# Kernel tuning notes

Hardware: AMD Instinct MI355X
Metric: run time of the kernel (lower is better)

The kernel has to match this reference:

```python
import jax, jax.numpy as jnp
import numpy as np

SEQ_LEN = 4096
N_FEATURES = 2048
N_HIDDEN = 2048
TAGS = 10
START_TAG = 8
STOP_TAG = 9
H = N_HIDDEN // 2  # per-direction hidden size


def setup_inputs() -> dict:
    key = jax.random.key(0)
    ks = jax.random.split(key, 10)
    s = 0.02
    sentence = jax.random.normal(ks[0], (SEQ_LEN, 1, N_FEATURES), jnp.float32)
    W_ih_f = jax.random.normal(ks[1], (4 * H, N_FEATURES), jnp.float32) * s
    W_hh_f = jax.random.normal(ks[2], (4 * H, H), jnp.float32) * s
    b_f = jax.random.normal(ks[3], (4 * H,), jnp.float32) * s
    W_ih_b = jax.random.normal(ks[4], (4 * H, N_FEATURES), jnp.float32) * s
    W_hh_b = jax.random.normal(ks[5], (4 * H, H), jnp.float32) * s
    b_b = jax.random.normal(ks[6], (4 * H,), jnp.float32) * s
    W_lin = jax.random.normal(ks[7], (TAGS, N_HIDDEN), jnp.float32) * s
    b_lin = jax.random.normal(ks[8], (TAGS,), jnp.float32) * s
    transitions = jax.random.normal(ks[9], (TAGS, TAGS), jnp.float32)
    transitions = transitions.at[START_TAG, :].set(-10000.0).at[:, STOP_TAG].set(-10000.0)
    return {"sentence": sentence, "W_ih_f": W_ih_f, "W_hh_f": W_hh_f, "b_f": b_f,
            "W_ih_b": W_ih_b, "W_hh_b": W_hh_b, "b_b": b_b,
            "W_lin": W_lin, "b_lin": b_lin, "transitions": transitions}


def _lstm_dir(x, W_ih, W_hh, b, reverse):
    # Precompute the input projection for all timesteps (one big GEMM).
    xp = jnp.einsum('tbf,gf->tbg', x, W_ih) + b  # [T, B, 4H]
    B = x.shape[1]
    init = (jnp.zeros((B, H), x.dtype), jnp.zeros((B, H), x.dtype))

    def step(carry, g):
        h, c = carry
        gates = g + h @ W_hh.T  # [B, 4H], PyTorch gate order i, f, g, o
        i, f, gg, o = jnp.split(gates, 4, axis=-1)
        c = jax.nn.sigmoid(f) * c + jax.nn.sigmoid(i) * jnp.tanh(gg)
        h = jax.nn.sigmoid(o) * jnp.tanh(c)
        return (h, c), h

    _, hs = jax.lax.scan(step, init, xp, reverse=reverse)
    return hs  # [T, B, H]


def reference(sentence, W_ih_f, W_hh_f, b_f, W_ih_b, W_hh_b, b_b, W_lin, b_lin, transitions):
    h_f = _lstm_dir(sentence, W_ih_f, W_hh_f, b_f, False)
    h_b = _lstm_dir(sentence, W_ih_b, W_hh_b, b_b, True)
    lstm_out = jnp.concatenate([h_f, h_b], axis=-1)         # [T, 1, N_HIDDEN]
    feats = lstm_out @ W_lin.T + b_lin                       # [T, 1, TAGS]
    f = feats[:, 0, :]                                       # [T, TAGS] (batch=1 as in original)

    init_v = jnp.full((TAGS,), -10000.0, f.dtype).at[START_TAG].set(0.0)

    def vstep(fv, feat):
        scores = fv[None, :] + transitions                   # [next_tag, prev_tag]
        return jnp.max(scores, axis=1) + feat, jnp.argmax(scores, axis=1)

    fv, bps = jax.lax.scan(vstep, init_v, f)                 # bps: [T, TAGS]
    terminal = fv + transitions[STOP_TAG]
    path_score = jnp.max(terminal)
    best_last = jnp.argmax(terminal)

    def bstep(tag, bp):
        return bp[tag], tag

    _, best_path = jax.lax.scan(bstep, best_last, bps, reverse=True)  # [T] in time order
    return path_score, best_path
```

## Files before the change

kernel.cpp:

```cpp
#include <hip/hip_runtime.h>

typedef _Float16 f16;
typedef _Float16 f16x4 __attribute__((ext_vector_type(4)));
typedef _Float16 f16x8 __attribute__((ext_vector_type(8)));
typedef float f32x4 __attribute__((ext_vector_type(4)));
typedef unsigned u32x4 __attribute__((ext_vector_type(4)));

#define SEQ 4096
#define NF  2048
#define HID 1024

__device__ f16   g_Ahi[SEQ * NF];
__device__ f16   g_Alo[SEQ * NF];
__device__ f16   g_Whi[2 * 4096 * NF];
__device__ f16   g_Wlo[2 * 4096 * NF];
__device__ float g_xp [2u * SEQ * 4096u];
__device__ float g_hist[2u * SEQ * HID];
__device__ unsigned long long g_ring[2][2][1024];
__device__ float g_feats[SEQ * 10];

__global__ void cvt_split(const float* __restrict__ src, int which, int n4) {
  int i = blockIdx.x * blockDim.x + threadIdx.x;
  int stride = gridDim.x * blockDim.x;
  f16* hi; f16* lo;
  if (which == 0)      { hi = g_Ahi; lo = g_Alo; }
  else if (which == 1) { hi = g_Whi; lo = g_Wlo; }
  else                 { hi = g_Whi + 4096 * NF; lo = g_Wlo + 4096 * NF; }
  const float4* s4 = (const float4*)src;
  f16x4* h4 = (f16x4*)hi;
  f16x4* l4 = (f16x4*)lo;
  for (int idx = i; idx < n4; idx += stride) {
    float4 v = s4[idx];
    f16x4 h, l;
    h.x = (f16)v.x; l.x = (f16)(v.x - (float)h.x);
    h.y = (f16)v.y; l.y = (f16)(v.y - (float)h.y);
    h.z = (f16)v.z; l.z = (f16)(v.z - (float)h.z);
    h.w = (f16)v.w; l.w = (f16)(v.w - (float)h.w);
    h4[idx] = h; l4[idx] = l;
  }
}

__global__ __launch_bounds__(256, 1) void gemm_xp(
    const float* __restrict__ b_f, const float* __restrict__ b_b)
{
  const int d = blockIdx.z;
  const f16* WhiD = g_Whi + (size_t)d * (4096u * 2048u);
  const f16* WloD = g_Wlo + (size_t)d * (4096u * 2048u);
  const float* bias = d ? b_b : b_f;
  float* out = g_xp + (size_t)d * (4096u * 4096u);

  __shared__ f16 sAh[128 * 40];
  __shared__ f16 sAl[128 * 40];
  __shared__ f16 sWh[128 * 40];
  __shared__ f16 sWl[128 * 40];

  const int tid  = threadIdx.x;
  const int lane = tid & 63;
  const int wv   = tid >> 6;
  const int quad = lane >> 4;
  const int mrow = lane & 15;
  const int m0 = (wv & 1) * 64;
  const int n0 = (wv >> 1) * 64;
  const int bm = blockIdx.y, bn = blockIdx.x;

  f32x4 acc[4][4] = {};

  const int r0  = tid >> 2;
  const int seg = tid & 3;

  for (int kt = 0; kt < 2048; kt += 32) {
#pragma unroll
    for (int r = 0; r < 2; ++r) {
      int row = r * 64 + r0;
      size_t ga = (size_t)(bm * 128 + row) * 2048 + kt + seg * 8;
      size_t gw = (size_t)(bn * 128 + row) * 2048 + kt + seg * 8;
      int lidx = row * 40 + seg * 8;
      *(f16x8*)&sAh[lidx] = *(const f16x8*)&g_Ahi[ga];
      *(f16x8*)&sAl[lidx] = *(const f16x8*)&g_Alo[ga];
      *(f16x8*)&sWh[lidx] = *(const f16x8*)&WhiD[gw];
      *(f16x8*)&sWl[lidx] = *(const f16x8*)&WloD[gw];
    }
    __syncthreads();

    f16x8 ah[4], al[4], wh[4], wl[4];
#pragma unroll
    for (int mi = 0; mi < 4; ++mi) {
      int rowm = (m0 + mi * 16 + mrow) * 40 + quad * 8;
      ah[mi] = *(const f16x8*)&sAh[rowm];
      al[mi] = *(const f16x8*)&sAl[rowm];
    }
#pragma unroll
    for (int ni = 0; ni < 4; ++ni) {
      int rown = (n0 + ni * 16 + mrow) * 40 + quad * 8;
      wh[ni] = *(const f16x8*)&sWh[rown];
      wl[ni] = *(const f16x8*)&sWl[rown];
    }
#pragma unroll
    for (int mi = 0; mi < 4; ++mi)
#pragma unroll
      for (int ni = 0; ni < 4; ++ni) {
        acc[mi][ni] = __builtin_amdgcn_mfma_f32_16x16x32_f16(ah[mi], wh[ni], acc[mi][ni], 0, 0, 0);
        acc[mi][ni] = __builtin_amdgcn_mfma_f32_16x16x32_f16(ah[mi], wl[ni], acc[mi][ni], 0, 0, 0);
        acc[mi][ni] = __builtin_amdgcn_mfma_f32_16x16x32_f16(al[mi], wh[ni], acc[mi][ni], 0, 0, 0);
      }
    __syncthreads();
  }

#pragma unroll
  for (int ni = 0; ni < 4; ++ni) {
    int g = bn * 128 + n0 + ni * 16 + mrow;
    float bv = bias[g];
#pragma unroll
    for (int mi = 0; mi < 4; ++mi) {
#pragma unroll
      for (int r = 0; r < 4; ++r) {
        int t = bm * 128 + m0 + mi * 16 + quad * 4 + r;
        out[(size_t)t * 4096 + g] = acc[mi][ni][r] + bv;
      }
    }
  }
}

__global__ void init_sync() {
  int i = blockIdx.x * blockDim.x + threadIdx.x;
  ((unsigned long long*)g_ring)[i] = 0ull;
}

__global__ __launch_bounds__(1024) void lstm_persistent(
    const float* __restrict__ Whh_f, const float* __restrict__ Whh_b)
{
  const int bid = blockIdx.x;
  const int dir = bid & 1;
  const int wsl = bid >> 1;
  const int tid = threadIdx.x;
  const int r   = tid >> 4;
  const int l16 = tid & 15;

  __shared__ float h_lds[1024];
  __shared__ float gates_lds[64];

  const float* Wd = dir ? Whh_b : Whh_f;

  const int grow = (r >> 4) * 1024 + wsl * 16 + (r & 15);
  float4 w4[16];
#pragma unroll
  for (int j = 0; j < 16; ++j)
    w4[j] = *(const float4*)&Wd[(size_t)grow * 1024 + 4 * l16 + 64 * j];

  const float* xpd = g_xp + (size_t)dir * 4096u * 4096u;
  float* histd = g_hist + (size_t)dir * 4096u * 1024u;

  float c = 0.f;

  for (int t = 1; t <= 4096; ++t) {
    const int tau = dir ? (4096 - t) : (t - 1);

    float xv0 = 0.f, xv1 = 0.f, xv2 = 0.f, xv3 = 0.f;
    if (tid < 16) {
      const float* px = xpd + (size_t)tau * 4096 + wsl * 16 + tid;
      xv0 = px[0]; xv1 = px[1024]; xv2 = px[2048]; xv3 = px[3072];
    }

    if (tid < 512) {
      const unsigned need = (unsigned)(t - 1);
      const unsigned long long* rs = &g_ring[dir][(t - 1) & 1][0] + 2 * tid;
      u32x4 q;
      for (;;) {
        asm volatile("global_load_dwordx4 %0, %1, off sc0 sc1\n\t"
                     "s_waitcnt vmcnt(0)"
                     : "=v"(q) : "v"(rs) : "memory");
        if (q.y == need && q.w == need) break;
        __builtin_amdgcn_s_sleep(1);
      }
      float2 hv;
      hv.x = __uint_as_float(q.x);
      hv.y = __uint_as_float(q.z);
      *(float2*)&h_lds[2 * tid] = hv;
    }
    __syncthreads();

    float p0 = 0.f, p1 = 0.f, p2 = 0.f, p3 = 0.f;
#pragma unroll
    for (int j = 0; j < 16; j += 4) {
      float4 h0 = *(const float4*)&h_lds[4 * l16 + 64 * (j + 0)];
      float4 h1 = *(const float4*)&h_lds[4 * l16 + 64 * (j + 1)];
      float4 h2 = *(const float4*)&h_lds[4 * l16 + 64 * (j + 2)];
      float4 h3 = *(const float4*)&h_lds[4 * l16 + 64 * (j + 3)];
      p0 += w4[j+0].x*h0.x + w4[j+0].y*h0.y + w4[j+0].z*h0.z + w4[j+0].w*h0.w;
      p1 += w4[j+1].x*h1.x + w4[j+1].y*h1.y + w4[j+1].z*h1.z + w4[j+1].w*h1.w;
      p2 += w4[j+2].x*h2.x + w4[j+2].y*h2.y + w4[j+2].z*h2.z + w4[j+2].w*h2.w;
      p3 += w4[j+3].x*h3.x + w4[j+3].y*h3.y + w4[j+3].z*h3.z + w4[j+3].w*h3.w;
    }
    float acc = (p0 + p1) + (p2 + p3);
    acc += __shfl_xor(acc, 1);
    acc += __shfl_xor(acc, 2);
    acc += __shfl_xor(acc, 4);
    acc += __shfl_xor(acc, 8);
    if (l16 == 0) gates_lds[r] = acc;
    __syncthreads();

    if (tid < 16) {
      float gi = gates_lds[tid]      + xv0;
      float gf = gates_lds[16 + tid] + xv1;
      float gg = gates_lds[32 + tid] + xv2;
      float go = gates_lds[48 + tid] + xv3;
      float si = 1.f / (1.f + __expf(-gi));
      float sf = 1.f / (1.f + __expf(-gf));
      float so = 1.f / (1.f + __expf(-go));
      float tg = 1.f - 2.f / (1.f + __expf(2.f * gg));
      c = sf * c + si * tg;
      float th = 1.f - 2.f / (1.f + __expf(2.f * c));
      float h  = so * th;
      histd[(size_t)tau * 1024 + wsl * 16 + tid] = h;
      unsigned long long pk = ((unsigned long long)(unsigned)t << 32)
                            | (unsigned long long)__float_as_uint(h);
      __hip_atomic_store(&g_ring[dir][t & 1][wsl * 16 + tid], pk,
                         __ATOMIC_RELAXED, __HIP_MEMORY_SCOPE_AGENT);
    }
  }
}

__global__ __launch_bounds__(256, 1) void feats_kernel(
    const float* __restrict__ W_lin, const float* __restrict__ b_lin)
{
  const int tid = threadIdx.x;
  const int wv = tid >> 6, l = tid & 63;
  const int t0 = blockIdx.x * 16 + wv * 4;
  for (int it = 0; it < 4; ++it) {
    const int t = t0 + it;
    float hf[16], hbv[16];
#pragma unroll
    for (int i = 0; i < 16; ++i) hf[i]  = g_hist[(size_t)t * 1024 + l + 64 * i];
#pragma unroll
    for (int i = 0; i < 16; ++i) hbv[i] = g_hist[(size_t)(4096 + t) * 1024 + l + 64 * i];
#pragma unroll
    for (int tag = 0; tag < 10; ++tag) {
      float a = 0.f;
#pragma unroll
      for (int i = 0; i < 16; ++i) {
        a += W_lin[tag * 2048 + l + 64 * i] * hf[i];
        a += W_lin[tag * 2048 + 1024 + l + 64 * i] * hbv[i];
      }
      a += __shfl_xor(a, 32); a += __shfl_xor(a, 16); a += __shfl_xor(a, 8);
      a += __shfl_xor(a, 4);  a += __shfl_xor(a, 2);  a += __shfl_xor(a, 1);
      if (l == 0) g_feats[t * 10 + tag] = a + b_lin[tag];
    }
  }
}

__global__ __launch_bounds__(64, 1) void viterbi_kernel(
    const float* __restrict__ trans, float* __restrict__ out)
{
  __shared__ unsigned char bps[4096 * 10];
  const int to = threadIdx.x;
  float tr[10];
#pragma unroll
  for (int f = 0; f < 10; ++f) tr[f] = (to < 10) ? trans[to * 10 + f] : 0.f;
  float fv = (to == 8) ? 0.f : -10000.f;

  float fbuf[8];
#pragma unroll
  for (int i = 0; i < 8; ++i) fbuf[i] = (to < 10) ? g_feats[i * 10 + to] : 0.f;

  for (int t = 0; t < 4096; t += 8) {
#pragma unroll
    for (int u = 0; u < 8; ++u) {
      const int tt = t + u;
      float m = -3.4e38f; int am = 0;
#pragma unroll
      for (int f = 0; f < 10; ++f) {
        float v = __shfl(fv, f) + tr[f];
        if (v > m) { m = v; am = f; }
      }
      float ft = fbuf[u];
      if (tt + 8 < 4096 && to < 10) fbuf[u] = g_feats[(tt + 8) * 10 + to];
      fv = m + ft;
      if (to < 10) bps[tt * 10 + to] = (unsigned char)am;
    }
  }
  __syncthreads();

  float term = fv + ((to < 10) ? trans[90 + to] : -3.4e38f);
  float best = -3.4e38f; int bl = 0;
#pragma unroll
  for (int f = 0; f < 10; ++f) {
    float v = __shfl(term, f);
    if (v > best) { best = v; bl = f; }
  }
  if (to == 0) {
    out[0] = best;
    int tag = bl;
    for (int t = 4095; t >= 0; --t) {
      out[1 + t] = (float)tag;
      tag = bps[t * 10 + tag];
    }
  }
}

extern "C" void kernel_launch(void* const* d_in, const int* in_sizes, int n_in,
                              void* d_out, int out_size, void* d_ws, size_t ws_size,
                              hipStream_t stream)
{
  (void)in_sizes; (void)n_in; (void)out_size; (void)d_ws; (void)ws_size;
  const float* W_hh_f   = (const float*)d_in[2];
  const float* b_f      = (const float*)d_in[3];
  const float* W_hh_b   = (const float*)d_in[5];
  const float* b_b      = (const float*)d_in[6];
  const float* W_lin    = (const float*)d_in[7];
  const float* b_lin    = (const float*)d_in[8];
  const float* trans    = (const float*)d_in[9];

  cvt_split<<<1024, 256, 0, stream>>>((const float*)d_in[0], 0, 2097152);
  cvt_split<<<1024, 256, 0, stream>>>((const float*)d_in[1], 1, 2097152);
  cvt_split<<<1024, 256, 0, stream>>>((const float*)d_in[4], 2, 2097152);

  gemm_xp<<<dim3(32, 32, 2), 256, 0, stream>>>(b_f, b_b);

  init_sync<<<16, 256, 0, stream>>>();

  lstm_persistent<<<128, 1024, 0, stream>>>(W_hh_f, W_hh_b);

  feats_kernel<<<256, 256, 0, stream>>>(W_lin, b_lin);

  viterbi_kernel<<<1, 64, 0, stream>>>(trans, (float*)d_out);
}
```

Before: 11.59 ms.

## Restructure persistent LSTM into 256 blocks of 512 threads with wave-local gate math

Splits the recurrent LSTM across 256 blocks of 512 threads. Each wave owns one hidden unit and holds all four of its gate rows, so the gate nonlinearity is done with wave shuffles and the second __syncthreads per step is gone. The h and xp LDS buffers are double-buffered, and every thread polls the global ring with two outstanding loads and a wave-wide __all check. The cost is twice as many blocks spinning on the agent-scope ring, and each block now handles fewer hidden units.

```diff
diff --git a/kernel.cpp b/kernel.cpp
--- a/kernel.cpp
+++ b/kernel.cpp
@@ -126,22 +126,24 @@
   ((unsigned long long*)g_ring)[i] = 0ull;
 }
 
-__global__ __launch_bounds__(1024) void lstm_persistent(
+__global__ __launch_bounds__(512) void lstm_persistent(
     const float* __restrict__ Whh_f, const float* __restrict__ Whh_b)
 {
-  const int bid = blockIdx.x;
-  const int dir = bid & 1;
-  const int wsl = bid >> 1;
-  const int tid = threadIdx.x;
-  const int r   = tid >> 4;
-  const int l16 = tid & 15;
-
-  __shared__ float h_lds[1024];
-  __shared__ float gates_lds[64];
-
-  const float* Wd = dir ? Whh_b : Whh_f;
-
-  const int grow = (r >> 4) * 1024 + wsl * 16 + (r & 15);
+  const int bid  = blockIdx.x;
+  const int dir  = bid & 1;
+  const int wsl  = bid >> 1;
+  const int tid  = threadIdx.x;
+  const int w    = tid >> 6;
+  const int gate = (tid >> 4) & 3;
+  const int l16  = tid & 15;
+
+  __shared__ float h_lds[2][1024];
+  __shared__ float xp_lds[2][32];
+
+  const float* Wd  = dir ? Whh_b : Whh_f;
+  const int dim  = wsl * 8 + w;
+  const int grow = gate * 1024 + dim;
+
   float4 w4[16];
 #pragma unroll
   for (int j = 0; j < 16; ++j)
@@ -149,73 +151,77 @@
 
   const float* xpd = g_xp + (size_t)dir * 4096u * 4096u;
   float* histd = g_hist + (size_t)dir * 4096u * 1024u;
+  unsigned long long* ringd = &g_ring[dir][0][0];
 
   float c = 0.f;
 
   for (int t = 1; t <= 4096; ++t) {
     const int tau = dir ? (4096 - t) : (t - 1);
-
-    float xv0 = 0.f, xv1 = 0.f, xv2 = 0.f, xv3 = 0.f;
-    if (tid < 16) {
-      const float* px = xpd + (size_t)tau * 4096 + wsl * 16 + tid;
-      xv0 = px[0]; xv1 = px[1024]; xv2 = px[2048]; xv3 = px[3072];
-    }
-
-    if (tid < 512) {
-      const unsigned need = (unsigned)(t - 1);
-      const unsigned long long* rs = &g_ring[dir][(t - 1) & 1][0] + 2 * tid;
-      u32x4 q;
-      for (;;) {
-        asm volatile("global_load_dwordx4 %0, %1, off sc0 sc1\n\t"
-                     "s_waitcnt vmcnt(0)"
-                     : "=v"(q) : "v"(rs) : "memory");
-        if (q.y == need && q.w == need) break;
-        __builtin_amdgcn_s_sleep(1);
-      }
-      float2 hv;
-      hv.x = __uint_as_float(q.x);
-      hv.y = __uint_as_float(q.z);
-      *(float2*)&h_lds[2 * tid] = hv;
-    }
+    const int b   = t & 1;
+
+    float xv = 0.f;
+    if (tid < 32)
+      xv = xpd[(size_t)tau * 4096 + (tid >> 3) * 1024 + wsl * 8 + (tid & 7)];
+
+    const unsigned need = (unsigned)(t - 1);
+    const unsigned long long* rs = ringd + (size_t)((t - 1) & 1) * 1024 + 2 * tid;
+    u32x4 qa, qb, q;
+    asm volatile("global_load_dwordx4 %0, %1, off sc0 sc1" : "=v"(qa) : "v"(rs) : "memory");
+    asm volatile("global_load_dwordx4 %0, %1, off sc0 sc1" : "=v"(qb) : "v"(rs) : "memory");
+    for (;;) {
+      asm volatile("s_waitcnt vmcnt(1)" ::: "memory");
+      if (__all(qa.y == need && qa.w == need)) { q = qa; break; }
+      asm volatile("global_load_dwordx4 %0, %1, off sc0 sc1" : "=v"(qa) : "v"(rs) : "memory");
+      asm volatile("s_waitcnt vmcnt(1)" ::: "memory");
+      if (__all(qb.y == need && qb.w == need)) { q = qb; break; }
+      asm volatile("global_load_dwordx4 %0, %1, off sc0 sc1" : "=v"(qb) : "v"(rs) : "memory");
+      __builtin_amdgcn_s_sleep(1);
+    }
+    asm volatile("s_waitcnt vmcnt(0)" ::: "memory");
+    asm volatile("" :: "v"(qa), "v"(qb));
+
+    float2 hv;
+    hv.x = __uint_as_float(q.x);
+    hv.y = __uint_as_float(q.z);
+    *(float2*)&h_lds[b][2 * tid] = hv;
+    if (tid < 32) xp_lds[b][tid] = xv;
     __syncthreads();
 
     float p0 = 0.f, p1 = 0.f, p2 = 0.f, p3 = 0.f;
 #pragma unroll
     for (int j = 0; j < 16; j += 4) {
-      float4 h0 = *(const float4*)&h_lds[4 * l16 + 64 * (j + 0)];
-      float4 h1 = *(const float4*)&h_lds[4 * l16 + 64 * (j + 1)];
-      float4 h2 = *(const float4*)&h_lds[4 * l16 + 64 * (j + 2)];
-      float4 h3 = *(const float4*)&h_lds[4 * l16 + 64 * (j + 3)];
+      float4 h0 = *(const float4*)&h_lds[b][4 * l16 + 64 * (j + 0)];
+      float4 h1 = *(const float4*)&h_lds[b][4 * l16 + 64 * (j + 1)];
+      float4 h2 = *(const float4*)&h_lds[b][4 * l16 + 64 * (j + 2)];
+      float4 h3 = *(const float4*)&h_lds[b][4 * l16 + 64 * (j + 3)];
       p0 += w4[j+0].x*h0.x + w4[j+0].y*h0.y + w4[j+0].z*h0.z + w4[j+0].w*h0.w;
       p1 += w4[j+1].x*h1.x + w4[j+1].y*h1.y + w4[j+1].z*h1.z + w4[j+1].w*h1.w;
       p2 += w4[j+2].x*h2.x + w4[j+2].y*h2.y + w4[j+2].z*h2.z + w4[j+2].w*h2.w;
       p3 += w4[j+3].x*h3.x + w4[j+3].y*h3.y + w4[j+3].z*h3.z + w4[j+3].w*h3.w;
     }
-    float acc = (p0 + p1) + (p2 + p3);
-    acc += __shfl_xor(acc, 1);
-    acc += __shfl_xor(acc, 2);
-    acc += __shfl_xor(acc, 4);
-    acc += __shfl_xor(acc, 8);
-    if (l16 == 0) gates_lds[r] = acc;
-    __syncthreads();
-
-    if (tid < 16) {
-      float gi = gates_lds[tid]      + xv0;
-      float gf = gates_lds[16 + tid] + xv1;
-      float gg = gates_lds[32 + tid] + xv2;
-      float go = gates_lds[48 + tid] + xv3;
-      float si = 1.f / (1.f + __expf(-gi));
-      float sf = 1.f / (1.f + __expf(-gf));
-      float so = 1.f / (1.f + __expf(-go));
-      float tg = 1.f - 2.f / (1.f + __expf(2.f * gg));
-      c = sf * c + si * tg;
-      float th = 1.f - 2.f / (1.f + __expf(2.f * c));
-      float h  = so * th;
-      histd[(size_t)tau * 1024 + wsl * 16 + tid] = h;
+    float val = (p0 + p1) + (p2 + p3);
+    val += __shfl_xor(val, 1);
+    val += __shfl_xor(val, 2);
+    val += __shfl_xor(val, 4);
+    val += __shfl_xor(val, 8);
+    val += xp_lds[b][gate * 8 + w];
+    float gi = __shfl(val, l16);
+    float gf = __shfl(val, l16 + 16);
+    float gg = __shfl(val, l16 + 32);
+    float go = __shfl(val, l16 + 48);
+    float si = 1.f / (1.f + __expf(-gi));
+    float sf = 1.f / (1.f + __expf(-gf));
+    float so = 1.f / (1.f + __expf(-go));
+    float tg = 1.f - 2.f / (1.f + __expf(2.f * gg));
+    c = sf * c + si * tg;
+    float th = 1.f - 2.f / (1.f + __expf(2.f * c));
+    float h  = so * th;
+    if ((tid & 63) == 0) {
       unsigned long long pk = ((unsigned long long)(unsigned)t << 32)
                             | (unsigned long long)__float_as_uint(h);
-      __hip_atomic_store(&g_ring[dir][t & 1][wsl * 16 + tid], pk,
+      __hip_atomic_store(&ringd[(size_t)b * 1024 + dim], pk,
                          __ATOMIC_RELAXED, __HIP_MEMORY_SCOPE_AGENT);
+      histd[(size_t)tau * 1024 + dim] = h;
     }
   }
 }
@@ -318,7 +324,7 @@
 
   init_sync<<<16, 256, 0, stream>>>();
 
-  lstm_persistent<<<128, 1024, 0, stream>>>(W_hh_f, W_hh_b);
+  lstm_persistent<<<256, 512, 0, stream>>>(W_hh_f, W_hh_b);
 
   feats_kernel<<<256, 256, 0, stream>>>(W_lin, b_lin);
 
```

Result: slower. 22.30 ms (+92.4%).

## Replace tagged 64-bit ring with sentinel-marked 8-slot float ring

Applied to the files above, without the earlier changes.

The inter-block hidden-state exchange used 64-bit words pairing each value with a step tag, so every poll read twice the data. Each slot now holds a plain float, and readiness is marked by invalidating slots with a NaN sentinel four steps ahead in an 8-deep ring. Pollers read four values per dwordx4 load with half as many threads, and the history store is moved after the ring publish. The risk is correctness: a computed h that equals the sentinel bit pattern would hang the wait, and the reuse distance has to stay safe against block skew.

```diff
diff --git a/kernel.cpp b/kernel.cpp
--- a/kernel.cpp
+++ b/kernel.cpp
@@ -9,6 +9,7 @@
 #define SEQ 4096
 #define NF  2048
 #define HID 1024
+#define SENT 0x7F800001u
 
 __device__ f16   g_Ahi[SEQ * NF];
 __device__ f16   g_Alo[SEQ * NF];
@@ -16,7 +17,7 @@
 __device__ f16   g_Wlo[2 * 4096 * NF];
 __device__ float g_xp [2u * SEQ * 4096u];
 __device__ float g_hist[2u * SEQ * HID];
-__device__ unsigned long long g_ring[2][2][1024];
+__device__ float g_ring[2][8][1024];
 __device__ float g_feats[SEQ * 10];
 
 __global__ void cvt_split(const float* __restrict__ src, int which, int n4) {
@@ -123,7 +124,8 @@
 
 __global__ void init_sync() {
   int i = blockIdx.x * blockDim.x + threadIdx.x;
-  ((unsigned long long*)g_ring)[i] = 0ull;
+  int slot = (i >> 10) & 7;
+  ((unsigned*)g_ring)[i] = (slot == 0) ? 0u : SENT;
 }
 
 __global__ __launch_bounds__(1024) void lstm_persistent(
@@ -149,6 +151,7 @@
 
   const float* xpd = g_xp + (size_t)dir * 4096u * 4096u;
   float* histd = g_hist + (size_t)dir * 4096u * 1024u;
+  float* ringd = &g_ring[dir][0][0];
 
   float c = 0.f;
 
@@ -161,21 +164,22 @@
       xv0 = px[0]; xv1 = px[1024]; xv2 = px[2048]; xv3 = px[3072];
     }
 
-    if (tid < 512) {
-      const unsigned need = (unsigned)(t - 1);
-      const unsigned long long* rs = &g_ring[dir][(t - 1) & 1][0] + 2 * tid;
+    if (tid < 256) {
+      const float* rs = ringd + (size_t)((t - 1) & 7) * 1024 + 4 * tid;
       u32x4 q;
       for (;;) {
         asm volatile("global_load_dwordx4 %0, %1, off sc0 sc1\n\t"
                      "s_waitcnt vmcnt(0)"
                      : "=v"(q) : "v"(rs) : "memory");
-        if (q.y == need && q.w == need) break;
+        if (q.x != SENT && q.y != SENT && q.z != SENT && q.w != SENT) break;
         __builtin_amdgcn_s_sleep(1);
       }
-      float2 hv;
+      float4 hv;
       hv.x = __uint_as_float(q.x);
-      hv.y = __uint_as_float(q.z);
-      *(float2*)&h_lds[2 * tid] = hv;
+      hv.y = __uint_as_float(q.y);
+      hv.z = __uint_as_float(q.z);
+      hv.w = __uint_as_float(q.w);
+      *(float4*)&h_lds[4 * tid] = hv;
     }
     __syncthreads();
 
@@ -211,11 +215,15 @@
       c = sf * c + si * tg;
       float th = 1.f - 2.f / (1.f + __expf(2.f * c));
       float h  = so * th;
-      histd[(size_t)tau * 1024 + wsl * 16 + tid] = h;
-      unsigned long long pk = ((unsigned long long)(unsigned)t << 32)
-                            | (unsigned long long)__float_as_uint(h);
-      __hip_atomic_store(&g_ring[dir][t & 1][wsl * 16 + tid], pk,
+      const int dim = wsl * 16 + tid;
+      __hip_atomic_store((unsigned*)&ringd[(size_t)(t & 7) * 1024 + dim],
+                         __float_as_uint(h),
                          __ATOMIC_RELAXED, __HIP_MEMORY_SCOPE_AGENT);
+      if (t + 4 <= 4096)
+        __hip_atomic_store((unsigned*)&ringd[(size_t)((t + 4) & 7) * 1024 + dim],
+                           SENT,
+                           __ATOMIC_RELAXED, __HIP_MEMORY_SCOPE_AGENT);
+      histd[(size_t)tau * 1024 + dim] = h;
     }
   }
 }
@@ -316,7 +324,7 @@
 
   gemm_xp<<<dim3(32, 32, 2), 256, 0, stream>>>(b_f, b_b);
 
-  init_sync<<<16, 256, 0, stream>>>();
+  init_sync<<<16, 1024, 0, stream>>>();
 
   lstm_persistent<<<128, 1024, 0, stream>>>(W_hh_f, W_hh_b);
 
```

Result: faster. 10.75 ms (-7.2%).
